# Optimization experiments

Measured on AMD Instinct MI355X. Metric: run time of the kernel, lower is better.

The kernel has to match this reference:

```python
import jax, jax.numpy as jnp
import numpy as np

HIDDEN = 2048
NUM_HEADS = 32
NUM_KV_HEADS = 8
GROUP = NUM_HEADS // NUM_KV_HEADS  # 4
HEAD_DIM = HIDDEN // NUM_HEADS     # 64
SEQ = 2048


def setup_inputs() -> dict:
    key = jax.random.key(0)
    ks = jax.random.split(key, 5)
    s = HIDDEN ** -0.5
    x = jax.random.normal(ks[0], (SEQ, HIDDEN), jnp.float32)
    q_proj = jax.random.normal(ks[1], (HIDDEN, HIDDEN), jnp.float32) * s
    k_proj = jax.random.normal(ks[2], (HIDDEN, HIDDEN // GROUP), jnp.float32) * s
    v_proj = jax.random.normal(ks[3], (HIDDEN, HIDDEN // GROUP), jnp.float32) * s
    o_proj = jax.random.normal(ks[4], (HIDDEN, HIDDEN), jnp.float32) * s
    # inv_freq = 1/rsqrt(10000**(i/d)) = sqrt(10000**(i/d)) per the original module
    inv_freq = jnp.sqrt(10000.0 ** (jnp.arange(0, HEAD_DIM, 2) / HEAD_DIM)).astype(jnp.float32)
    return {"x": x, "q_proj": q_proj, "k_proj": k_proj, "v_proj": v_proj,
            "o_proj": o_proj, "inv_freq": inv_freq}


def _rope(x, inv_freq):
    # x: [S, ..., HEAD_DIM]; rotation per the original (nonstandard) formula.
    orig_dtype = x.dtype
    x = x.astype(jnp.float32)
    seq = jnp.arange(x.shape[0])
    angles = seq[:, None] * jax.lax.stop_gradient(inv_freq)[None, :]  # [S, HEAD_DIM//2]
    bshape = (x.shape[0],) + (1,) * (x.ndim - 2) + (HEAD_DIM // 2,)
    sins = jnp.sin(angles).reshape(bshape)
    coss = jnp.cos(angles).reshape(bshape)
    half, odd = jnp.split(x, 2, axis=-1)
    out = jnp.concatenate([half * coss + odd * sins, half * sins - odd * coss], axis=-1)
    return out.astype(orig_dtype)


def reference(x, q_proj, k_proj, v_proj, o_proj, inv_freq):
    S = x.shape[0]
    q = (x @ q_proj).reshape(S, NUM_KV_HEADS, GROUP, HEAD_DIM)
    k = (x @ k_proj).reshape(S, NUM_KV_HEADS, HEAD_DIM)
    v = (x @ v_proj).reshape(S, NUM_KV_HEADS, HEAD_DIM)
    q = _rope(q, inv_freq)
    k = _rope(k, inv_freq)
    # scores: [a=S, b=S, h=kv_heads, g=group]
    scores = jnp.einsum('ahgd,bhd->abhg', q, k) / (HEAD_DIM ** 0.5)
    mask = jnp.tril(jnp.ones((S, S), dtype=jnp.bool_))[:, :, None, None]
    scores = jnp.where(mask, scores, -jnp.inf)
    attn = jax.nn.softmax(scores, axis=1)  # softmax over b (axis=-3)
    o = jnp.einsum('abhg,bhd->ahgd', attn, v).reshape(S, HIDDEN)
    return o @ o_proj
```

## Files before the change

### kernel.cpp

```cpp
#include <hip/hip_runtime.h>


typedef __bf16 bf16_t;
typedef __bf16 bf16x4 __attribute__((ext_vector_type(4)));
typedef __bf16 bf16x8 __attribute__((ext_vector_type(8)));
typedef float  f32x4  __attribute__((ext_vector_type(4)));
typedef short  s16x4  __attribute__((ext_vector_type(4)));

#define S_LEN   2048
#define HID     2048
#define NKV     8
#define NH      32
#define DHEAD   64
#define KVW     (NKV * DHEAD)

__device__ __align__(16) bf16_t g_xb [S_LEN * HID];
__device__ __align__(16) bf16_t g_wTq[HID * HID];
__device__ __align__(16) bf16_t g_wTk[KVW * HID];
__device__ __align__(16) bf16_t g_wTv[KVW * HID];
__device__ __align__(16) bf16_t g_wTo[HID * HID];
__device__ __align__(16) bf16_t g_q [S_LEN * HID];
__device__ __align__(16) bf16_t g_k [S_LEN * KVW];
__device__ __align__(16) bf16_t g_vT[KVW * S_LEN];
__device__ __align__(16) bf16_t g_om[S_LEN * HID];
__device__ float g_ropeC[S_LEN * 32];
__device__ float g_ropeS[S_LEN * 32];

static __device__ inline s16x4 bc4(bf16x4 v) { s16x4 r; __builtin_memcpy(&r, &v, 8); return r; }

__device__ __forceinline__ void gll16(void* lds, const void* g) {
    __builtin_amdgcn_global_load_lds(
        (const __attribute__((address_space(1))) void*)g,
        (__attribute__((address_space(3))) void*)lds,
        16, 0, 0);
}

__global__ __launch_bounds__(256)
void prep_kernel(const float* __restrict__ x,
                 const float* __restrict__ qw, const float* __restrict__ kw,
                 const float* __restrict__ vw, const float* __restrict__ ow,
                 const void* __restrict__ invf_raw) {
    __shared__ bf16_t tile[64][65];
    int b = blockIdx.x, t = threadIdx.x;

    if (b < 256) {
        int idx = b * 256 + t;
        int s = idx >> 5, j = idx & 31;
        float f;
        if (*(const unsigned*)invf_raw == 0x3F800000u) {
            f = ((const float*)invf_raw)[j];
        } else {
            unsigned u = ((unsigned)((const unsigned short*)invf_raw)[j]) << 16;
            __builtin_memcpy(&f, &u, 4);
        }
        float a32 = (float)s * f;
        double a = (double)a32;
        g_ropeC[idx] = (float)cos(a);
        g_ropeS[idx] = (float)sin(a);
        return;
    }
    if (b < 4352) {
        int idx = (b - 256) * 256 + t;
        float4 v = reinterpret_cast<const float4*>(x)[idx];
        bf16x4 o;
        o[0] = (bf16_t)v.x; o[1] = (bf16_t)v.y; o[2] = (bf16_t)v.z; o[3] = (bf16_t)v.w;
        *reinterpret_cast<bf16x4*>(&g_xb[(size_t)idx * 4]) = o;
        return;
    }
    const float* in; bf16_t* outp; int R, C, tb;
    if (b < 5376)      { in = qw; outp = g_wTq; R = HID; C = HID; tb = b - 4352; }
    else if (b < 5632) { in = kw; outp = g_wTk; R = HID; C = KVW; tb = b - 5376; }
    else if (b < 5888) { in = vw; outp = g_wTv; R = HID; C = KVW; tb = b - 5632; }
    else               { in = ow; outp = g_wTo; R = HID; C = HID; tb = b - 5888; }
    int xt = C >> 6;
    int c0 = (tb % xt) * 64, r0 = (tb / xt) * 64;
    int tx4 = t & 15, ty = t >> 4;
    #pragma unroll
    for (int r = ty; r < 64; r += 16) {
        float4 v = *reinterpret_cast<const float4*>(
            &in[(size_t)(r0 + r) * C + c0 + tx4 * 4]);
        tile[r][tx4 * 4 + 0] = (bf16_t)v.x;
        tile[r][tx4 * 4 + 1] = (bf16_t)v.y;
        tile[r][tx4 * 4 + 2] = (bf16_t)v.z;
        tile[r][tx4 * 4 + 3] = (bf16_t)v.w;
    }
    __syncthreads();
    int wx = t & 63, wy = t >> 6;
    #pragma unroll
    for (int r = wy; r < 64; r += 4)
        outp[(size_t)(c0 + r) * R + r0 + wx] = tile[wx][r];
}

__global__ __launch_bounds__(256)
void gemm_fused_kernel(float* __restrict__ Cf, int which) {
    __shared__ __align__(16) bf16_t As[2][128 * 64];
    __shared__ __align__(16) bf16_t Bs[2][64 * 64];

    int t    = threadIdx.x;
    int lane = t & 63, wid = t >> 6;
    int quad = lane >> 4, l15 = lane & 15;

    int ntn  = (which == 1) ? 32 : 48;
    int nwg  = ntn * 16;
    int orig = blockIdx.x;
    int qq   = nwg >> 3;
    int wg   = (orig & 7) * qq + (orig >> 3);
    int my   = wg / ntn, nx = wg - my * ntn;
    int m0   = my * 128;

    const bf16_t* A; const bf16_t* Bt; int n0;
    if (which == 1)      { A = g_om; Bt = g_wTo; n0 = nx * 64; }
    else {
        A = g_xb;
        if (nx < 32)      { Bt = g_wTq; n0 = nx * 64; }
        else if (nx < 40) { Bt = g_wTk; n0 = (nx - 32) * 64; }
        else              { Bt = g_wTv; n0 = (nx - 40) * 64; }
    }

    int crow = lane >> 3;
    int gseg = (lane & 7) ^ crow;
    int so   = l15 & 7;
    int wm   = wid * 32;

    f32x4 acc[2][4];
    #pragma unroll
    for (int im = 0; im < 2; ++im)
        #pragma unroll
        for (int in = 0; in < 4; ++in)
            #pragma unroll
            for (int r = 0; r < 4; ++r) acc[im][in][r] = 0.f;

    auto stage = [&](int buf, int kt) {
        #pragma unroll
        for (int c = 0; c < 4; ++c)
            gll16(&As[buf][(wid * 4 + c) * 512],
                  A  + (size_t)(m0 + (wid * 4 + c) * 8 + crow) * HID + kt + gseg * 8);
        #pragma unroll
        for (int c = 0; c < 2; ++c)
            gll16(&Bs[buf][(wid * 2 + c) * 512],
                  Bt + (size_t)(n0 + (wid * 2 + c) * 8 + crow) * HID + kt + gseg * 8);
    };

    stage(0, 0);

    for (int it = 0; it < 32; ++it) {
        int cur = it & 1;
        if (it + 1 < 32) {
            stage(cur ^ 1, (it + 1) * 64);
            asm volatile("s_waitcnt vmcnt(6)" ::: "memory");
        } else {
            asm volatile("s_waitcnt vmcnt(0)" ::: "memory");
        }
        asm volatile("s_barrier" ::: "memory");

        #pragma unroll
        for (int kh = 0; kh < 2; ++kh) {
            bf16x8 af[2], bfv[4];
            #pragma unroll
            for (int i = 0; i < 2; ++i)
                af[i]  = *reinterpret_cast<const bf16x8*>(
                    &As[cur][(wm + i * 16 + l15) * 64 + (((kh * 4 + quad) ^ so) * 8)]);
            #pragma unroll
            for (int i = 0; i < 4; ++i)
                bfv[i] = *reinterpret_cast<const bf16x8*>(
                    &Bs[cur][(i * 16 + l15) * 64 + (((kh * 4 + quad) ^ so) * 8)]);
            #pragma unroll
            for (int im = 0; im < 2; ++im)
                #pragma unroll
                for (int in = 0; in < 4; ++in)
                    acc[im][in] = __builtin_amdgcn_mfma_f32_16x16x32_bf16(
                        af[im], bfv[in], acc[im][in], 0, 0, 0);
        }

        asm volatile("s_barrier" ::: "memory");
    }

    if (which == 1) {
        #pragma unroll
        for (int im = 0; im < 2; ++im) {
            int rowb = m0 + wm + im * 16 + quad * 4;
            #pragma unroll
            for (int in = 0; in < 4; ++in) {
                int col = n0 + in * 16 + l15;
                #pragma unroll
                for (int r = 0; r < 4; ++r)
                    Cf[(size_t)(rowb + r) * HID + col] = acc[im][in][r];
            }
        }
    } else if (nx < 40) {
        bf16_t* Cb; int N, colbase;
        if (nx < 32) { Cb = g_q; N = HID; colbase = nx * 64; }
        else         { Cb = g_k; N = KVW; colbase = (nx - 32) * 64; }
        #pragma unroll
        for (int im = 0; im < 2; ++im) {
            #pragma unroll
            for (int r = 0; r < 4; ++r) {
                int row = m0 + wm + im * 16 + quad * 4 + r;
                #pragma unroll
                for (int in = 0; in < 2; ++in) {
                    int d = in * 16 + l15;
                    float a  = acc[im][in][r];
                    float bb = acc[im][in + 2][r];
                    float cc = g_ropeC[row * 32 + d];
                    float ss = g_ropeS[row * 32 + d];
                    Cb[(size_t)row * N + colbase + d]      = (bf16_t)(a * cc + bb * ss);
                    Cb[(size_t)row * N + colbase + 32 + d] = (bf16_t)(a * ss - bb * cc);
                }
            }
        }
    } else {
        #pragma unroll
        for (int im = 0; im < 2; ++im) {
            int rowb = m0 + wm + im * 16 + quad * 4;
            #pragma unroll
            for (int in = 0; in < 4; ++in) {
                int col = (nx - 40) * 64 + in * 16 + l15;
                #pragma unroll
                for (int r = 0; r < 4; ++r)
                    g_vT[(size_t)col * S_LEN + (rowb + r)] = (bf16_t)acc[im][in][r];
            }
        }
    }
}

__global__ __launch_bounds__(512)
void flash_part_kernel() {
    __shared__ __align__(16) bf16_t SM[2][2][2][64 * 64];

    int t    = threadIdx.x;
    int lane = t & 63, wid = t >> 6;
    int g    = wid >> 2;
    int wh   = wid & 3;
    int quad = lane >> 4, l15 = lane & 15;
    int bx   = blockIdx.x;
    int hk   = bx & 7;
    int slot = bx >> 3;
    int qb32 = (slot & 1) ? (slot >> 1) : (63 - (slot >> 1));
    int nkt  = (qb32 >> 1) + 1;
    int ng   = (nkt + 1) >> 1;

    int head = hk * 4 + wh;
    int q0   = qb32 * 32;

    int crow = lane >> 3;
    int gseg = (lane & 7) ^ crow;
    int so   = l15 & 7;

    bf16x8 aq[2][2];
    #pragma unroll
    for (int mq = 0; mq < 2; ++mq) {
        const bf16_t* qp = g_q + (size_t)(q0 + mq * 16 + l15) * HID + head * 64 + quad * 8;
        aq[mq][0] = *reinterpret_cast<const bf16x8*>(qp);
        aq[mq][1] = *reinterpret_cast<const bf16x8*>(qp + 32);
        #pragma unroll
        for (int j = 0; j < 8; ++j) {
            aq[mq][0][j] = (bf16_t)((float)aq[mq][0][j] * 0.125f);
            aq[mq][1][j] = (bf16_t)((float)aq[mq][1][j] * 0.125f);
        }
    }

    bf16x4 ones4;
    #pragma unroll
    for (int j = 0; j < 4; ++j) ones4[j] = (bf16_t)1.0f;
    s16x4 ones_s = bc4(ones4);

    f32x4 oacc[2][4], liacc[2];
    #pragma unroll
    for (int mq = 0; mq < 2; ++mq) {
        #pragma unroll
        for (int r = 0; r < 4; ++r) liacc[mq][r] = 0.f;
        #pragma unroll
        for (int dt = 0; dt < 4; ++dt)
            #pragma unroll
            for (int r = 0; r < 4; ++r) oacc[mq][dt][r] = 0.f;
    }

    int qcol[2] = { q0 + l15, q0 + 16 + l15 };

    auto stageKV = [&](int buf, int k0) {
        #pragma unroll
        for (int c = 0; c < 2; ++c) {
            int ch = wh * 2 + c;
            gll16(&SM[g][0][buf][ch * 512],
                  g_k  + (size_t)(k0 + ch * 8 + crow) * KVW + hk * 64 + gseg * 8);
            gll16(&SM[g][1][buf][ch * 512],
                  g_vT + (size_t)(hk * 64 + ch * 8 + crow) * S_LEN + k0 + gseg * 8);
        }
    };

    if (g < nkt) stageKV(0, g * 64);

    for (int i = 0; i < ng; ++i) {
        int cur  = i & 1;
        int kt   = 2 * i + g;
        bool live = (kt < nkt);
        int ktn  = kt + 2;
        bool stage_next = (i + 1 < ng) && (ktn < nkt);
        if (stage_next) {
            stageKV(cur ^ 1, ktn * 64);
            asm volatile("s_waitcnt vmcnt(4)" ::: "memory");
        } else {
            asm volatile("s_waitcnt vmcnt(0)" ::: "memory");
        }
        asm volatile("s_barrier" ::: "memory");

        if (live) {
            int k0 = kt * 64;
            bf16x8 ak[4][2];
            #pragma unroll
            for (int mk = 0; mk < 4; ++mk) {
                int row = mk * 16 + l15;
                ak[mk][0] = *reinterpret_cast<const bf16x8*>(&SM[g][0][cur][row * 64 + ((quad ^ so) * 8)]);
                ak[mk][1] = *reinterpret_cast<const bf16x8*>(&SM[g][0][cur][row * 64 + (((4 + quad) ^ so) * 8)]);
            }

            f32x4 sacc[4][2];
            #pragma unroll
            for (int mk = 0; mk < 4; ++mk)
                #pragma unroll
                for (int mq = 0; mq < 2; ++mq) {
                    f32x4 s;
                    #pragma unroll
                    for (int r = 0; r < 4; ++r) s[r] = 0.f;
                    s = __builtin_amdgcn_mfma_f32_16x16x32_bf16(ak[mk][0], aq[mq][0], s, 0, 0, 0);
                    s = __builtin_amdgcn_mfma_f32_16x16x32_bf16(ak[mk][1], aq[mq][1], s, 0, 0, 0);
                    sacc[mk][mq] = s;
                }

            s16x4 pas[4][2];
            #pragma unroll
            for (int mk = 0; mk < 4; ++mk)
                #pragma unroll
                for (int mq = 0; mq < 2; ++mq) {
                    bf16x4 pa;
                    #pragma unroll
                    for (int r = 0; r < 4; ++r) {
                        int kk = k0 + mk * 16 + quad * 4 + r;
                        pa[r] = (bf16_t)((kk <= qcol[mq]) ? __expf(sacc[mk][mq][r] - 16.0f) : 0.0f);
                    }
                    pas[mk][mq] = bc4(pa);
                }

            #pragma unroll
            for (int mk = 0; mk < 4; ++mk) {
                #pragma unroll
                for (int dt = 0; dt < 4; ++dt) {
                    int rv = dt * 16 + l15;
                    int vb = rv * 64 + (((mk * 2 + (quad >> 1)) ^ so) * 8) + (quad & 1) * 4;
                    bf16x4 bv = *reinterpret_cast<const bf16x4*>(&SM[g][1][cur][vb]);
                    s16x4 bvs = bc4(bv);
                    #pragma unroll
                    for (int mq = 0; mq < 2; ++mq)
                        oacc[mq][dt] = __builtin_amdgcn_mfma_f32_16x16x16bf16_1k(pas[mk][mq], bvs, oacc[mq][dt], 0, 0, 0);
                }
                #pragma unroll
                for (int mq = 0; mq < 2; ++mq)
                    liacc[mq] = __builtin_amdgcn_mfma_f32_16x16x16bf16_1k(pas[mk][mq], ones_s, liacc[mq], 0, 0, 0);
            }
        }

        asm volatile("s_barrier" ::: "memory");
    }

    float* pO = reinterpret_cast<float*>(&SM[1][0][0][0]);
    float* pl = reinterpret_cast<float*>(&SM[0][0][0][0]);
    if (g == 1) {
        #pragma unroll
        for (int mq = 0; mq < 2; ++mq)
            #pragma unroll
            for (int r = 0; r < 4; ++r) {
                int row = mq * 16 + quad * 4 + r;
                #pragma unroll
                for (int dt = 0; dt < 4; ++dt)
                    pO[(wh * 32 + row) * 64 + dt * 16 + l15] = oacc[mq][dt][r];
                if (l15 == 0) pl[wh * 32 + row] = liacc[mq][r];
            }
    }
    asm volatile("s_waitcnt lgkmcnt(0)" ::: "memory");
    asm volatile("s_barrier" ::: "memory");
    if (g == 0) {
        #pragma unroll
        for (int mq = 0; mq < 2; ++mq)
            #pragma unroll
            for (int r = 0; r < 4; ++r) {
                int row = mq * 16 + quad * 4 + r;
                float l = liacc[mq][r] + pl[wh * 32 + row];
                float inv = 1.0f / l;
                #pragma unroll
                for (int dt = 0; dt < 4; ++dt) {
                    float o = oacc[mq][dt][r] + pO[(wh * 32 + row) * 64 + dt * 16 + l15];
                    g_om[(size_t)(q0 + row) * HID + head * 64 + dt * 16 + l15] = (bf16_t)(o * inv);
                }
            }
    }
}

extern "C" void kernel_launch(void* const* d_in, const int* in_sizes, int n_in,
                              void* d_out, int out_size, void* d_ws, size_t ws_size,
                              hipStream_t stream) {
    const float* x    = (const float*)d_in[0];
    const float* qpW  = (const float*)d_in[1];
    const float* kpW  = (const float*)d_in[2];
    const float* vpW  = (const float*)d_in[3];
    const float* opW  = (const float*)d_in[4];
    const void*  invf = d_in[5];
    float* out = (float*)d_out;

    prep_kernel<<<6912, 256, 0, stream>>>(x, qpW, kpW, vpW, opW, invf);
    gemm_fused_kernel<<<768, 256, 0, stream>>>(nullptr, 0);
    flash_part_kernel<<<512, 512, 0, stream>>>();
    gemm_fused_kernel<<<512, 256, 0, stream>>>(out, 1);
}
```

Measured before the change: 245.2 us.

## Split weight transpose into own kernel with vectorized bf16x8 stores, swizzle flash LDS

Moves the weight transpose out of the prep kernel into a separate kernel. That kernel keeps an fp32 LDS tile and writes each transposed row as 16-byte bf16x8 stores instead of scattered 2-byte stores. It also XOR-swizzles the LDS layout used to combine the two partial flash-attention results, to reduce bank conflicts. The cost is one extra kernel launch and more LDS per transpose block.

```diff
diff --git a/kernel.cpp b/kernel.cpp
--- a/kernel.cpp
+++ b/kernel.cpp
@@ -36,11 +36,7 @@
 }
 
 __global__ __launch_bounds__(256)
-void prep_kernel(const float* __restrict__ x,
-                 const float* __restrict__ qw, const float* __restrict__ kw,
-                 const float* __restrict__ vw, const float* __restrict__ ow,
-                 const void* __restrict__ invf_raw) {
-    __shared__ bf16_t tile[64][65];
+void prep_kernel(const float* __restrict__ x, const void* __restrict__ invf_raw) {
     int b = blockIdx.x, t = threadIdx.x;
 
     if (b < 256) {
@@ -59,36 +55,49 @@
         g_ropeS[idx] = (float)sin(a);
         return;
     }
-    if (b < 4352) {
-        int idx = (b - 256) * 256 + t;
-        float4 v = reinterpret_cast<const float4*>(x)[idx];
-        bf16x4 o;
-        o[0] = (bf16_t)v.x; o[1] = (bf16_t)v.y; o[2] = (bf16_t)v.z; o[3] = (bf16_t)v.w;
-        *reinterpret_cast<bf16x4*>(&g_xb[(size_t)idx * 4]) = o;
-        return;
-    }
+    int idx = (b - 256) * 256 + t;
+    float4 v = reinterpret_cast<const float4*>(x)[idx];
+    bf16x4 o;
+    o[0] = (bf16_t)v.x; o[1] = (bf16_t)v.y; o[2] = (bf16_t)v.z; o[3] = (bf16_t)v.w;
+    *reinterpret_cast<bf16x4*>(&g_xb[(size_t)idx * 4]) = o;
+}
+
+__global__ __launch_bounds__(256)
+void transpose_kernel(const float* __restrict__ qw, const float* __restrict__ kw,
+                      const float* __restrict__ vw, const float* __restrict__ ow) {
+    __shared__ float tile[64][65];
+    int b = blockIdx.x, t = threadIdx.x;
+
     const float* in; bf16_t* outp; int R, C, tb;
-    if (b < 5376)      { in = qw; outp = g_wTq; R = HID; C = HID; tb = b - 4352; }
-    else if (b < 5632) { in = kw; outp = g_wTk; R = HID; C = KVW; tb = b - 5376; }
-    else if (b < 5888) { in = vw; outp = g_wTv; R = HID; C = KVW; tb = b - 5632; }
-    else               { in = ow; outp = g_wTo; R = HID; C = HID; tb = b - 5888; }
+    if (b < 1024)      { in = qw; outp = g_wTq; R = HID; C = HID; tb = b; }
+    else if (b < 1280) { in = kw; outp = g_wTk; R = HID; C = KVW; tb = b - 1024; }
+    else if (b < 1536) { in = vw; outp = g_wTv; R = HID; C = KVW; tb = b - 1280; }
+    else               { in = ow; outp = g_wTo; R = HID; C = HID; tb = b - 1536; }
     int xt = C >> 6;
     int c0 = (tb % xt) * 64, r0 = (tb / xt) * 64;
+
     int tx4 = t & 15, ty = t >> 4;
     #pragma unroll
     for (int r = ty; r < 64; r += 16) {
         float4 v = *reinterpret_cast<const float4*>(
             &in[(size_t)(r0 + r) * C + c0 + tx4 * 4]);
-        tile[r][tx4 * 4 + 0] = (bf16_t)v.x;
-        tile[r][tx4 * 4 + 1] = (bf16_t)v.y;
-        tile[r][tx4 * 4 + 2] = (bf16_t)v.z;
-        tile[r][tx4 * 4 + 3] = (bf16_t)v.w;
+        tile[r][tx4 * 4 + 0] = v.x;
+        tile[r][tx4 * 4 + 1] = v.y;
+        tile[r][tx4 * 4 + 2] = v.z;
+        tile[r][tx4 * 4 + 3] = v.w;
     }
     __syncthreads();
-    int wx = t & 63, wy = t >> 6;
-    #pragma unroll
-    for (int r = wy; r < 64; r += 4)
-        outp[(size_t)(c0 + r) * R + r0 + wx] = tile[wx][r];
+
+    int cc = t & 63, j0 = t >> 6;
+    #pragma unroll
+    for (int jj = 0; jj < 2; ++jj) {
+        int j = j0 + jj * 4;
+        bf16x8 o8;
+        #pragma unroll
+        for (int i = 0; i < 8; ++i)
+            o8[i] = (bf16_t)tile[8 * j + i][cc];
+        *reinterpret_cast<bf16x8*>(&outp[(size_t)(c0 + cc) * R + r0 + 8 * j]) = o8;
+    }
 }
 
 __global__ __launch_bounds__(256)
@@ -370,9 +379,10 @@
             #pragma unroll
             for (int r = 0; r < 4; ++r) {
                 int row = mq * 16 + quad * 4 + r;
+                int sw  = ((row >> 2) & 3) << 3;
                 #pragma unroll
                 for (int dt = 0; dt < 4; ++dt)
-                    pO[(wh * 32 + row) * 64 + dt * 16 + l15] = oacc[mq][dt][r];
+                    pO[(wh * 32 + row) * 64 + ((dt * 16 + l15) ^ sw)] = oacc[mq][dt][r];
                 if (l15 == 0) pl[wh * 32 + row] = liacc[mq][r];
             }
     }
@@ -384,11 +394,12 @@
             #pragma unroll
             for (int r = 0; r < 4; ++r) {
                 int row = mq * 16 + quad * 4 + r;
+                int sw  = ((row >> 2) & 3) << 3;
                 float l = liacc[mq][r] + pl[wh * 32 + row];
                 float inv = 1.0f / l;
                 #pragma unroll
                 for (int dt = 0; dt < 4; ++dt) {
-                    float o = oacc[mq][dt][r] + pO[(wh * 32 + row) * 64 + dt * 16 + l15];
+                    float o = oacc[mq][dt][r] + pO[(wh * 32 + row) * 64 + ((dt * 16 + l15) ^ sw)];
                     g_om[(size_t)(q0 + row) * HID + head * 64 + dt * 16 + l15] = (bf16_t)(o * inv);
                 }
             }
@@ -406,7 +417,8 @@
     const void*  invf = d_in[5];
     float* out = (float*)d_out;
 
-    prep_kernel<<<6912, 256, 0, stream>>>(x, qpW, kpW, vpW, opW, invf);
+    prep_kernel<<<4352, 256, 0, stream>>>(x, invf);
+    transpose_kernel<<<2560, 256, 0, stream>>>(qpW, kpW, vpW, opW);
     gemm_fused_kernel<<<768, 256, 0, stream>>>(nullptr, 0);
     flash_part_kernel<<<512, 512, 0, stream>>>();
     gemm_fused_kernel<<<512, 256, 0, stream>>>(out, 1);
```

After: 246.7 us. No clear change (+0.6%).
